# Performance work log

Measured on AMD Instinct MI355X. Metric: run time of the kernel, lower is better.

Reference implementation:

```python
import jax, jax.numpy as jnp
import numpy as np

N = 2048

def setup_inputs() -> dict:
    key = jax.random.key(0)
    k0, k1, k2, k3 = jax.random.split(key, 4)
    return {
        "input": jax.random.normal(k0, (N, N), dtype=jnp.float32),
        "weight1": jax.random.normal(k1, (N, N), dtype=jnp.float32),
        "weight2": jax.random.normal(k2, (N, N), dtype=jnp.float32),
        "weight3": jax.random.normal(k3, (N, N), dtype=jnp.float32),
    }

def reference(input, weight1, weight2, weight3):
    # Faithful translation of the torch DAG (duplicate mm kept: t4 == t2,
    # so t8 is mathematically zero, but we preserve the original math).
    t1 = input @ weight1
    t2 = input @ weight2
    t3 = weight3 @ weight3
    t4 = input @ weight2
    t5 = t1 * weight1
    t6 = (t5 @ input) * weight1
    t7 = t1 * t2 + t1 + t3
    t8 = t2 - t4
    t9 = t7 * t8 + t6 * t3
    t11 = t3 * t9
    t12 = t3 * (t1 @ input) * t6
    t13 = t7 + t11
    t14 = t8 + t12
    t15 = t13 + t14
    return t15
```

## Files before the change

### kernel.cpp

```cpp
#include <hip/hip_runtime.h>
#include <hip/hip_bf16.h>
#include <stdint.h>

#define NN 2048
#define BK 32

typedef __bf16 bf16;
typedef __bf16 bf16x8 __attribute__((ext_vector_type(8)));
typedef __bf16 bf16x4 __attribute__((ext_vector_type(4)));
typedef float f32x4 __attribute__((ext_vector_type(4)));

__device__ __forceinline__ void async_copy16(bf16* lds, const bf16* g) {
    __builtin_amdgcn_global_load_lds(
        (const __attribute__((address_space(1))) unsigned int*)g,
        (__attribute__((address_space(3))) unsigned int*)lds,
        16, 0, 0);
}

#define WAIT_VM(n) asm volatile("s_waitcnt vmcnt(" #n ")" ::: "memory")
#define BAR()                                  \
    do {                                       \
        asm volatile("" ::: "memory");         \
        __builtin_amdgcn_s_barrier();          \
        asm volatile("" ::: "memory");         \
    } while (0)

struct CastArgs {
    const float* in[4];
    bf16*        outT[4];
    bf16*        outN[4];
};

__global__ __launch_bounds__(256) void transpose_cast_kernel(CastArgs args) {
    const float* __restrict__ in = args.in[blockIdx.z];
    bf16* __restrict__ outT      = args.outT[blockIdx.z];
    bf16* __restrict__ outN      = args.outN[blockIdx.z];
    __shared__ float tile[64][65];
    const int bx = blockIdx.x * 64;
    const int by = blockIdx.y * 64;
    const int t  = threadIdx.x;
    const int tc = t & 15, tr = t >> 4;
#pragma unroll
    for (int p = 0; p < 4; ++p) {
        const int r = tr + p * 16;
        const float4 v = *(const float4*)&in[(size_t)(by + r) * NN + bx + tc * 4];
        tile[r][tc * 4 + 0] = v.x; tile[r][tc * 4 + 1] = v.y;
        tile[r][tc * 4 + 2] = v.z; tile[r][tc * 4 + 3] = v.w;
        if (outN) {
            bf16x4 b = {(bf16)v.x, (bf16)v.y, (bf16)v.z, (bf16)v.w};
            *(bf16x4*)&outN[(size_t)(by + r) * NN + bx + tc * 4] = b;
        }
    }
    __syncthreads();
    const int cc = t >> 2, e = t & 3;
#pragma unroll
    for (int u = 0; u < 2; ++u) {
        const int r0 = e * 16 + u * 8;
        bf16x8 b;
#pragma unroll
        for (int i = 0; i < 8; ++i) b[i] = (bf16)tile[r0 + i][cc];
        *(bf16x8*)&outT[(size_t)(bx + cc) * NN + by + r0] = b;
    }
}

struct Gemm3Args {
    const bf16*  A[3];
    const bf16*  Bt[3];
    float*       C[3];
    const float* W1;
    bf16*        M1bf;
    bf16*        B1bf;
};

__global__ __launch_bounds__(256) void gemm3_kernel(Gemm3Args args) {
    const bf16* __restrict__ A  = args.A[blockIdx.z];
    const bf16* __restrict__ Bt = args.Bt[blockIdx.z];
    float* __restrict__ C       = args.C[blockIdx.z];

    __shared__ bf16 As0[128 * BK], As1[128 * BK], As2[128 * BK];
    __shared__ bf16 Bs0[128 * BK], Bs1[128 * BK], Bs2[128 * BK];

    const int t  = threadIdx.x;
    const int bm = blockIdx.x * 128;
    const int bn = blockIdx.y * 128;

    const int row0 = t >> 2;
    const int qp   = t & 3;
    const int col0 = ((qp ^ ((row0 >> 1) & 3)) << 3);
    const int off0 = t * 8;

    const bf16* gA0 = A  + (size_t)(bm + row0) * NN + col0;
    const bf16* gB0 = Bt + (size_t)(bn + row0) * NN + col0;

    const int wave = t >> 6;
    const int lane = t & 63;
    const int wm   = (wave >> 1) * 64;
    const int wn   = (wave & 1) * 64;
    const int lrow = lane & 15;
    const int q    = lane >> 4;
    const int qe   = (q ^ ((lrow >> 1) & 3)) << 3;

    f32x4 acc[4][4];
#pragma unroll
    for (int i = 0; i < 4; ++i)
#pragma unroll
        for (int j = 0; j < 4; ++j) acc[i][j] = (f32x4){0.f, 0.f, 0.f, 0.f};

    auto issue = [&](bf16* As, bf16* Bs, int kt) {
        const int kof = kt * BK;
        async_copy16(&As[off0],           gA0 + kof);
        async_copy16(&As[off0 + 64 * BK], gA0 + (size_t)64 * NN + kof);
        async_copy16(&Bs[off0],           gB0 + kof);
        async_copy16(&Bs[off0 + 64 * BK], gB0 + (size_t)64 * NN + kof);
    };
    auto compute = [&](const bf16* As, const bf16* Bs) {
        bf16x8 af[4], bfr[4];
#pragma unroll
        for (int i = 0; i < 4; ++i)
            af[i] = *(const bf16x8*)&As[(wm + i * 16 + lrow) * BK + qe];
#pragma unroll
        for (int j = 0; j < 4; ++j)
            bfr[j] = *(const bf16x8*)&Bs[(wn + j * 16 + lrow) * BK + qe];
#pragma unroll
        for (int i = 0; i < 4; ++i)
#pragma unroll
            for (int j = 0; j < 4; ++j)
                acc[i][j] = __builtin_amdgcn_mfma_f32_16x16x32_bf16(
                    af[i], bfr[j], acc[i][j], 0, 0, 0);
    };

    issue(As0, Bs0, 0);
    issue(As1, Bs1, 1);
#pragma unroll 1
    for (int kt = 0; kt < 60; kt += 3) {
        issue(As2, Bs2, kt + 2); WAIT_VM(8); BAR(); compute(As0, Bs0); BAR();
        issue(As0, Bs0, kt + 3); WAIT_VM(8); BAR(); compute(As1, Bs1); BAR();
        issue(As1, Bs1, kt + 4); WAIT_VM(8); BAR(); compute(As2, Bs2); BAR();
    }
    issue(As2, Bs2, 62); WAIT_VM(8); BAR(); compute(As0, Bs0); BAR();
    issue(As0, Bs0, 63); WAIT_VM(8); BAR(); compute(As1, Bs1); BAR();
    WAIT_VM(4); BAR(); compute(As2, Bs2); BAR();
    WAIT_VM(0); BAR(); compute(As0, Bs0);

    const int z = blockIdx.z;
#pragma unroll
    for (int i = 0; i < 4; ++i)
#pragma unroll
        for (int j = 0; j < 4; ++j)
#pragma unroll
            for (int r = 0; r < 4; ++r) {
                const size_t idx = (size_t)(bm + wm + i * 16 + q * 4 + r) * NN +
                                   (bn + wn + j * 16 + lrow);
                const float v = acc[i][j][r];
                C[idx] = v;
                if (z == 0) {
                    const float w = args.W1[idx];
                    args.M1bf[idx] = (bf16)v;
                    args.B1bf[idx] = (bf16)(v * w);
                }
            }
}

struct Gemm2Args {
    const bf16*  M1bf;
    const bf16*  B1bf;
    const bf16*  At;
    const float* M1;
    const float* M3;
    const float* W1;
    float*       out;
};

__global__ __launch_bounds__(256) void gemm2_fused_kernel(Gemm2Args args) {
    __shared__ bf16 A50[128 * BK], A51[128 * BK], A52[128 * BK];
    __shared__ bf16 A40[128 * BK], A41[128 * BK], A42[128 * BK];
    __shared__ bf16 Bs0[64 * BK],  Bs1[64 * BK],  Bs2[64 * BK];

    const int t  = threadIdx.x;
    const int bm = blockIdx.x * 128;
    const int bn = blockIdx.y * 64;

    const int row0 = t >> 2;
    const int qp   = t & 3;
    const int col0 = ((qp ^ ((row0 >> 1) & 3)) << 3);
    const int off0 = t * 8;

    const bf16* g5 = args.M1bf + (size_t)(bm + row0) * NN + col0;
    const bf16* g4 = args.B1bf + (size_t)(bm + row0) * NN + col0;
    const bf16* gB = args.At   + (size_t)(bn + row0) * NN + col0;

    const int wave = t >> 6;
    const int lane = t & 63;
    const int wm   = (wave >> 1) * 64;
    const int wn   = (wave & 1) * 32;
    const int lrow = lane & 15;
    const int q    = lane >> 4;
    const int qe   = (q ^ ((lrow >> 1) & 3)) << 3;

    f32x4 acc5[4][2], acc4[4][2];
#pragma unroll
    for (int i = 0; i < 4; ++i)
#pragma unroll
        for (int j = 0; j < 2; ++j) {
            acc5[i][j] = (f32x4){0.f, 0.f, 0.f, 0.f};
            acc4[i][j] = (f32x4){0.f, 0.f, 0.f, 0.f};
        }

    auto issue = [&](bf16* A5, bf16* A4, bf16* Bs, int kt) {
        const int kof = kt * BK;
        async_copy16(&A5[off0],           g5 + kof);
        async_copy16(&A5[off0 + 64 * BK], g5 + (size_t)64 * NN + kof);
        async_copy16(&A4[off0],           g4 + kof);
        async_copy16(&A4[off0 + 64 * BK], g4 + (size_t)64 * NN + kof);
        async_copy16(&Bs[off0],           gB + kof);
    };
    auto compute = [&](const bf16* A5, const bf16* A4, const bf16* Bs) {
        bf16x8 a5[4], a4[4], bfr[2];
#pragma unroll
        for (int i = 0; i < 4; ++i) {
            a5[i] = *(const bf16x8*)&A5[(wm + i * 16 + lrow) * BK + qe];
            a4[i] = *(const bf16x8*)&A4[(wm + i * 16 + lrow) * BK + qe];
        }
#pragma unroll
        for (int j = 0; j < 2; ++j)
            bfr[j] = *(const bf16x8*)&Bs[(wn + j * 16 + lrow) * BK + qe];
#pragma unroll
        for (int i = 0; i < 4; ++i)
#pragma unroll
            for (int j = 0; j < 2; ++j) {
                acc5[i][j] = __builtin_amdgcn_mfma_f32_16x16x32_bf16(
                    a5[i], bfr[j], acc5[i][j], 0, 0, 0);
                acc4[i][j] = __builtin_amdgcn_mfma_f32_16x16x32_bf16(
                    a4[i], bfr[j], acc4[i][j], 0, 0, 0);
            }
    };

    issue(A50, A40, Bs0, 0);
    issue(A51, A41, Bs1, 1);
#pragma unroll 1
    for (int kt = 0; kt < 60; kt += 3) {
        issue(A52, A42, Bs2, kt + 2); WAIT_VM(10); BAR(); compute(A50, A40, Bs0); BAR();
        issue(A50, A40, Bs0, kt + 3); WAIT_VM(10); BAR(); compute(A51, A41, Bs1); BAR();
        issue(A51, A41, Bs1, kt + 4); WAIT_VM(10); BAR(); compute(A52, A42, Bs2); BAR();
    }
    issue(A52, A42, Bs2, 62); WAIT_VM(10); BAR(); compute(A50, A40, Bs0); BAR();
    issue(A50, A40, Bs0, 63); WAIT_VM(10); BAR(); compute(A51, A41, Bs1); BAR();
    WAIT_VM(5); BAR(); compute(A52, A42, Bs2); BAR();
    WAIT_VM(0); BAR(); compute(A50, A40, Bs0);

#pragma unroll
    for (int i = 0; i < 4; ++i)
#pragma unroll
        for (int j = 0; j < 2; ++j)
#pragma unroll
            for (int r = 0; r < 4; ++r) {
                const size_t idx = (size_t)(bm + wm + i * 16 + q * 4 + r) * NN +
                                   (bn + wn + j * 16 + lrow);
                const float m5 = acc5[i][j][r];
                const float m4 = acc4[i][j][r];
                const float m1 = args.M1[idx];
                const float m3 = args.M3[idx];
                const float w1 = args.W1[idx];
                const float m2 = args.out[idx];
                args.out[idx] =
                    m1 * m2 + m1 + m3 + m3 * (m4 * w1) * (m3 + m5);
            }
}

extern "C" void kernel_launch(void* const* d_in, const int* in_sizes, int n_in,
                              void* d_out, int out_size, void* d_ws, size_t ws_size,
                              hipStream_t stream) {
    const float* A  = (const float*)d_in[0];
    const float* W1 = (const float*)d_in[1];
    const float* W2 = (const float*)d_in[2];
    const float* W3 = (const float*)d_in[3];
    float* out = (float*)d_out;

    const size_t P = (size_t)NN * NN;
    char* ws = (char*)d_ws;

    bf16* Abf  = (bf16*)ws;
    bf16* At   = Abf + P;
    bf16* W1t  = At + P;
    bf16* W2t  = W1t + P;
    bf16* W3bf = W2t + P;
    bf16* W3t  = W3bf + P;
    bf16* M1bf = W3t + P;
    bf16* B1bf = M1bf + P;
    float* M1  = (float*)(B1bf + P);
    float* M3  = M1 + P;

    CastArgs ca;
    ca.in[0] = A;  ca.outT[0] = At;  ca.outN[0] = Abf;
    ca.in[1] = W1; ca.outT[1] = W1t; ca.outN[1] = nullptr;
    ca.in[2] = W2; ca.outT[2] = W2t; ca.outN[2] = nullptr;
    ca.in[3] = W3; ca.outT[3] = W3t; ca.outN[3] = W3bf;
    transpose_cast_kernel<<<dim3(NN / 64, NN / 64, 4), 256, 0, stream>>>(ca);

    Gemm3Args g3;
    g3.A[0] = Abf;  g3.Bt[0] = W1t; g3.C[0] = M1;
    g3.A[1] = Abf;  g3.Bt[1] = W2t; g3.C[1] = out;
    g3.A[2] = W3bf; g3.Bt[2] = W3t; g3.C[2] = M3;
    g3.W1 = W1; g3.M1bf = M1bf; g3.B1bf = B1bf;
    gemm3_kernel<<<dim3(NN / 128, NN / 128, 3), 256, 0, stream>>>(g3);

    Gemm2Args g2;
    g2.M1bf = M1bf; g2.B1bf = B1bf; g2.At = At;
    g2.M1 = M1; g2.M3 = M3; g2.W1 = W1; g2.out = out;
    gemm2_fused_kernel<<<dim3(NN / 128, NN / 64), 256, 0, stream>>>(g2);
}
```

Before: 258.6 us.

## Merge A@W1 and A@W2 GEMMs sharing A tiles; double-buffer and retile phase kernels

The first GEMM phase now computes input@W1 and input@W2 in one block, so each A tile loaded into LDS feeds two B operands. The W3@W3 product runs as a separate z-slice. Both paths move from triple to double buffering and request two blocks per CU via launch_bounds. The second fused GEMM gives each wave a 32x64 tile instead of 64x32, and the transpose-cast kernel changes its LDS read pattern on the transposed write side. This cuts A-tile global traffic but leaves the z=0 and z=1 blocks with unequal work (two accumulators versus one), which can cause load imbalance and higher register pressure.

```diff
diff --git a/kernel.cpp b/kernel.cpp
--- a/kernel.cpp
+++ b/kernel.cpp
@@ -39,46 +39,48 @@
     const int bx = blockIdx.x * 64;
     const int by = blockIdx.y * 64;
     const int t  = threadIdx.x;
-    const int tc = t & 15, tr = t >> 4;
+    const int c4 = (t & 15) * 4, r0 = t >> 4;
 #pragma unroll
     for (int p = 0; p < 4; ++p) {
-        const int r = tr + p * 16;
-        const float4 v = *(const float4*)&in[(size_t)(by + r) * NN + bx + tc * 4];
-        tile[r][tc * 4 + 0] = v.x; tile[r][tc * 4 + 1] = v.y;
-        tile[r][tc * 4 + 2] = v.z; tile[r][tc * 4 + 3] = v.w;
+        const int r = r0 + p * 16;
+        const float4 v = *(const float4*)&in[(size_t)(by + r) * NN + bx + c4];
+        tile[r][c4 + 0] = v.x; tile[r][c4 + 1] = v.y;
+        tile[r][c4 + 2] = v.z; tile[r][c4 + 3] = v.w;
         if (outN) {
             bf16x4 b = {(bf16)v.x, (bf16)v.y, (bf16)v.z, (bf16)v.w};
-            *(bf16x4*)&outN[(size_t)(by + r) * NN + bx + tc * 4] = b;
+            *(bf16x4*)&outN[(size_t)(by + r) * NN + bx + c4] = b;
         }
     }
     __syncthreads();
-    const int cc = t >> 2, e = t & 3;
-#pragma unroll
-    for (int u = 0; u < 2; ++u) {
-        const int r0 = e * 16 + u * 8;
+    const int cc8 = (t & 7) * 8, rw0 = t >> 3;
+#pragma unroll
+    for (int p = 0; p < 2; ++p) {
+        const int rw = rw0 + p * 32;
         bf16x8 b;
 #pragma unroll
-        for (int i = 0; i < 8; ++i) b[i] = (bf16)tile[r0 + i][cc];
-        *(bf16x8*)&outT[(size_t)(bx + cc) * NN + by + r0] = b;
+        for (int i = 0; i < 8; ++i) b[i] = (bf16)tile[cc8 + i][rw];
+        *(bf16x8*)&outT[(size_t)(bx + rw) * NN + by + cc8] = b;
     }
 }
 
-struct Gemm3Args {
-    const bf16*  A[3];
-    const bf16*  Bt[3];
-    float*       C[3];
+struct P1Args {
+    const bf16*  Abf;
+    const bf16*  W1t;
+    const bf16*  W2t;
+    const bf16*  W3bf;
+    const bf16*  W3t;
+    float*       M1;
+    float*       M2out;
+    float*       M3;
     const float* W1;
     bf16*        M1bf;
     bf16*        B1bf;
 };
 
-__global__ __launch_bounds__(256) void gemm3_kernel(Gemm3Args args) {
-    const bf16* __restrict__ A  = args.A[blockIdx.z];
-    const bf16* __restrict__ Bt = args.Bt[blockIdx.z];
-    float* __restrict__ C       = args.C[blockIdx.z];
-
-    __shared__ bf16 As0[128 * BK], As1[128 * BK], As2[128 * BK];
-    __shared__ bf16 Bs0[128 * BK], Bs1[128 * BK], Bs2[128 * BK];
+__global__ __launch_bounds__(256, 2) void phase1_kernel(P1Args a) {
+    __shared__ bf16 As0[128 * BK], As1[128 * BK];
+    __shared__ bf16 B10[128 * BK], B11[128 * BK];
+    __shared__ bf16 B20[128 * BK], B21[128 * BK];
 
     const int t  = threadIdx.x;
     const int bm = blockIdx.x * 128;
@@ -88,9 +90,6 @@
     const int qp   = t & 3;
     const int col0 = ((qp ^ ((row0 >> 1) & 3)) << 3);
     const int off0 = t * 8;
-
-    const bf16* gA0 = A  + (size_t)(bm + row0) * NN + col0;
-    const bf16* gB0 = Bt + (size_t)(bn + row0) * NN + col0;
 
     const int wave = t >> 6;
     const int lane = t & 63;
@@ -100,65 +99,134 @@
     const int q    = lane >> 4;
     const int qe   = (q ^ ((lrow >> 1) & 3)) << 3;
 
-    f32x4 acc[4][4];
-#pragma unroll
-    for (int i = 0; i < 4; ++i)
-#pragma unroll
-        for (int j = 0; j < 4; ++j) acc[i][j] = (f32x4){0.f, 0.f, 0.f, 0.f};
-
-    auto issue = [&](bf16* As, bf16* Bs, int kt) {
-        const int kof = kt * BK;
-        async_copy16(&As[off0],           gA0 + kof);
-        async_copy16(&As[off0 + 64 * BK], gA0 + (size_t)64 * NN + kof);
-        async_copy16(&Bs[off0],           gB0 + kof);
-        async_copy16(&Bs[off0 + 64 * BK], gB0 + (size_t)64 * NN + kof);
-    };
-    auto compute = [&](const bf16* As, const bf16* Bs) {
-        bf16x8 af[4], bfr[4];
+    if (blockIdx.z == 0) {
+        const bf16* gA  = a.Abf + (size_t)(bm + row0) * NN + col0;
+        const bf16* gB1 = a.W1t + (size_t)(bn + row0) * NN + col0;
+        const bf16* gB2 = a.W2t + (size_t)(bn + row0) * NN + col0;
+
+        f32x4 acc1[4][4], acc2[4][4];
 #pragma unroll
         for (int i = 0; i < 4; ++i)
-            af[i] = *(const bf16x8*)&As[(wm + i * 16 + lrow) * BK + qe];
-#pragma unroll
-        for (int j = 0; j < 4; ++j)
-            bfr[j] = *(const bf16x8*)&Bs[(wn + j * 16 + lrow) * BK + qe];
+#pragma unroll
+            for (int j = 0; j < 4; ++j) {
+                acc1[i][j] = (f32x4){0.f, 0.f, 0.f, 0.f};
+                acc2[i][j] = (f32x4){0.f, 0.f, 0.f, 0.f};
+            }
+
+        auto issue = [&](bf16* As, bf16* B1, bf16* B2, int kt) {
+            const int kof = kt * BK;
+            async_copy16(&As[off0],           gA  + kof);
+            async_copy16(&As[off0 + 64 * BK], gA  + (size_t)64 * NN + kof);
+            async_copy16(&B1[off0],           gB1 + kof);
+            async_copy16(&B1[off0 + 64 * BK], gB1 + (size_t)64 * NN + kof);
+            async_copy16(&B2[off0],           gB2 + kof);
+            async_copy16(&B2[off0 + 64 * BK], gB2 + (size_t)64 * NN + kof);
+        };
+        auto compute = [&](const bf16* As, const bf16* B1, const bf16* B2) {
+            bf16x8 af[4], b1[4], b2[4];
+#pragma unroll
+            for (int i = 0; i < 4; ++i)
+                af[i] = *(const bf16x8*)&As[(wm + i * 16 + lrow) * BK + qe];
+#pragma unroll
+            for (int j = 0; j < 4; ++j) {
+                b1[j] = *(const bf16x8*)&B1[(wn + j * 16 + lrow) * BK + qe];
+                b2[j] = *(const bf16x8*)&B2[(wn + j * 16 + lrow) * BK + qe];
+            }
+#pragma unroll
+            for (int i = 0; i < 4; ++i)
+#pragma unroll
+                for (int j = 0; j < 4; ++j) {
+                    acc1[i][j] = __builtin_amdgcn_mfma_f32_16x16x32_bf16(
+                        af[i], b1[j], acc1[i][j], 0, 0, 0);
+                    acc2[i][j] = __builtin_amdgcn_mfma_f32_16x16x32_bf16(
+                        af[i], b2[j], acc2[i][j], 0, 0, 0);
+                }
+        };
+
+        issue(As0, B10, B20, 0);
+#pragma unroll 1
+        for (int kt = 0; kt < 62; kt += 2) {
+            issue(As1, B11, B21, kt + 1); WAIT_VM(6); BAR();
+            compute(As0, B10, B20); BAR();
+            issue(As0, B10, B20, kt + 2); WAIT_VM(6); BAR();
+            compute(As1, B11, B21); BAR();
+        }
+        issue(As1, B11, B21, 63); WAIT_VM(6); BAR();
+        compute(As0, B10, B20); BAR();
+        WAIT_VM(0); BAR();
+        compute(As1, B11, B21);
+
 #pragma unroll
         for (int i = 0; i < 4; ++i)
 #pragma unroll
             for (int j = 0; j < 4; ++j)
-                acc[i][j] = __builtin_amdgcn_mfma_f32_16x16x32_bf16(
-                    af[i], bfr[j], acc[i][j], 0, 0, 0);
-    };
-
-    issue(As0, Bs0, 0);
-    issue(As1, Bs1, 1);
+#pragma unroll
+                for (int r = 0; r < 4; ++r) {
+                    const size_t idx =
+                        (size_t)(bm + wm + i * 16 + q * 4 + r) * NN +
+                        (bn + wn + j * 16 + lrow);
+                    const float v1 = acc1[i][j][r];
+                    a.M1[idx]    = v1;
+                    a.M2out[idx] = acc2[i][j][r];
+                    const float w = a.W1[idx];
+                    a.M1bf[idx] = (bf16)v1;
+                    a.B1bf[idx] = (bf16)(v1 * w);
+                }
+    } else {
+        const bf16* gA = a.W3bf + (size_t)(bm + row0) * NN + col0;
+        const bf16* gB = a.W3t  + (size_t)(bn + row0) * NN + col0;
+
+        f32x4 acc[4][4];
+#pragma unroll
+        for (int i = 0; i < 4; ++i)
+#pragma unroll
+            for (int j = 0; j < 4; ++j) acc[i][j] = (f32x4){0.f, 0.f, 0.f, 0.f};
+
+        auto issue = [&](bf16* As, bf16* Bs, int kt) {
+            const int kof = kt * BK;
+            async_copy16(&As[off0],           gA + kof);
+            async_copy16(&As[off0 + 64 * BK], gA + (size_t)64 * NN + kof);
+            async_copy16(&Bs[off0],           gB + kof);
+            async_copy16(&Bs[off0 + 64 * BK], gB + (size_t)64 * NN + kof);
+        };
+        auto compute = [&](const bf16* As, const bf16* Bs) {
+            bf16x8 af[4], bfr[4];
+#pragma unroll
+            for (int i = 0; i < 4; ++i)
+                af[i] = *(const bf16x8*)&As[(wm + i * 16 + lrow) * BK + qe];
+#pragma unroll
+            for (int j = 0; j < 4; ++j)
+                bfr[j] = *(const bf16x8*)&Bs[(wn + j * 16 + lrow) * BK + qe];
+#pragma unroll
+            for (int i = 0; i < 4; ++i)
+#pragma unroll
+                for (int j = 0; j < 4; ++j)
+                    acc[i][j] = __builtin_amdgcn_mfma_f32_16x16x32_bf16(
+                        af[i], bfr[j], acc[i][j], 0, 0, 0);
+        };
+
+        issue(As0, B10, 0);
 #pragma unroll 1
-    for (int kt = 0; kt < 60; kt += 3) {
-        issue(As2, Bs2, kt + 2); WAIT_VM(8); BAR(); compute(As0, Bs0); BAR();
-        issue(As0, Bs0, kt + 3); WAIT_VM(8); BAR(); compute(As1, Bs1); BAR();
-        issue(As1, Bs1, kt + 4); WAIT_VM(8); BAR(); compute(As2, Bs2); BAR();
+        for (int kt = 0; kt < 62; kt += 2) {
+            issue(As1, B11, kt + 1); WAIT_VM(4); BAR();
+            compute(As0, B10); BAR();
+            issue(As0, B10, kt + 2); WAIT_VM(4); BAR();
+            compute(As1, B11); BAR();
+        }
+        issue(As1, B11, 63); WAIT_VM(4); BAR();
+        compute(As0, B10); BAR();
+        WAIT_VM(0); BAR();
+        compute(As1, B11);
+
+#pragma unroll
+        for (int i = 0; i < 4; ++i)
+#pragma unroll
+            for (int j = 0; j < 4; ++j)
+#pragma unroll
+                for (int r = 0; r < 4; ++r)
+                    a.M3[(size_t)(bm + wm + i * 16 + q * 4 + r) * NN +
+                         (bn + wn + j * 16 + lrow)] = acc[i][j][r];
     }
-    issue(As2, Bs2, 62); WAIT_VM(8); BAR(); compute(As0, Bs0); BAR();
-    issue(As0, Bs0, 63); WAIT_VM(8); BAR(); compute(As1, Bs1); BAR();
-    WAIT_VM(4); BAR(); compute(As2, Bs2); BAR();
-    WAIT_VM(0); BAR(); compute(As0, Bs0);
-
-    const int z = blockIdx.z;
-#pragma unroll
-    for (int i = 0; i < 4; ++i)
-#pragma unroll
-        for (int j = 0; j < 4; ++j)
-#pragma unroll
-            for (int r = 0; r < 4; ++r) {
-                const size_t idx = (size_t)(bm + wm + i * 16 + q * 4 + r) * NN +
-                                   (bn + wn + j * 16 + lrow);
-                const float v = acc[i][j][r];
-                C[idx] = v;
-                if (z == 0) {
-                    const float w = args.W1[idx];
-                    args.M1bf[idx] = (bf16)v;
-                    args.B1bf[idx] = (bf16)(v * w);
-                }
-            }
 }
 
 struct Gemm2Args {
@@ -171,7 +239,7 @@
     float*       out;
 };
 
-__global__ __launch_bounds__(256) void gemm2_fused_kernel(Gemm2Args args) {
+__global__ __launch_bounds__(256, 2) void gemm2_fused_kernel(Gemm2Args args) {
     __shared__ bf16 A50[128 * BK], A51[128 * BK], A52[128 * BK];
     __shared__ bf16 A40[128 * BK], A41[128 * BK], A42[128 * BK];
     __shared__ bf16 Bs0[64 * BK],  Bs1[64 * BK],  Bs2[64 * BK];
@@ -191,17 +259,16 @@
 
     const int wave = t >> 6;
     const int lane = t & 63;
-    const int wm   = (wave >> 1) * 64;
-    const int wn   = (wave & 1) * 32;
+    const int wm   = wave * 32;
     const int lrow = lane & 15;
     const int q    = lane >> 4;
     const int qe   = (q ^ ((lrow >> 1) & 3)) << 3;
 
-    f32x4 acc5[4][2], acc4[4][2];
-#pragma unroll
-    for (int i = 0; i < 4; ++i)
-#pragma unroll
-        for (int j = 0; j < 2; ++j) {
+    f32x4 acc5[2][4], acc4[2][4];
+#pragma unroll
+    for (int i = 0; i < 2; ++i)
+#pragma unroll
+        for (int j = 0; j < 4; ++j) {
             acc5[i][j] = (f32x4){0.f, 0.f, 0.f, 0.f};
             acc4[i][j] = (f32x4){0.f, 0.f, 0.f, 0.f};
         }
@@ -215,19 +282,19 @@
         async_copy16(&Bs[off0],           gB + kof);
     };
     auto compute = [&](const bf16* A5, const bf16* A4, const bf16* Bs) {
-        bf16x8 a5[4], a4[4], bfr[2];
-#pragma unroll
-        for (int i = 0; i < 4; ++i) {
+        bf16x8 a5[2], a4[2], bfr[4];
+#pragma unroll
+        for (int i = 0; i < 2; ++i) {
             a5[i] = *(const bf16x8*)&A5[(wm + i * 16 + lrow) * BK + qe];
             a4[i] = *(const bf16x8*)&A4[(wm + i * 16 + lrow) * BK + qe];
         }
 #pragma unroll
-        for (int j = 0; j < 2; ++j)
-            bfr[j] = *(const bf16x8*)&Bs[(wn + j * 16 + lrow) * BK + qe];
-#pragma unroll
-        for (int i = 0; i < 4; ++i)
-#pragma unroll
-            for (int j = 0; j < 2; ++j) {
+        for (int j = 0; j < 4; ++j)
+            bfr[j] = *(const bf16x8*)&Bs[(j * 16 + lrow) * BK + qe];
+#pragma unroll
+        for (int i = 0; i < 2; ++i)
+#pragma unroll
+            for (int j = 0; j < 4; ++j) {
                 acc5[i][j] = __builtin_amdgcn_mfma_f32_16x16x32_bf16(
                     a5[i], bfr[j], acc5[i][j], 0, 0, 0);
                 acc4[i][j] = __builtin_amdgcn_mfma_f32_16x16x32_bf16(
@@ -249,13 +316,13 @@
     WAIT_VM(0); BAR(); compute(A50, A40, Bs0);
 
 #pragma unroll
-    for (int i = 0; i < 4; ++i)
-#pragma unroll
-        for (int j = 0; j < 2; ++j)
+    for (int i = 0; i < 2; ++i)
+#pragma unroll
+        for (int j = 0; j < 4; ++j)
 #pragma unroll
             for (int r = 0; r < 4; ++r) {
                 const size_t idx = (size_t)(bm + wm + i * 16 + q * 4 + r) * NN +
-                                   (bn + wn + j * 16 + lrow);
+                                   (bn + j * 16 + lrow);
                 const float m5 = acc5[i][j][r];
                 const float m4 = acc4[i][j][r];
                 const float m1 = args.M1[idx];
@@ -297,12 +364,11 @@
     ca.in[3] = W3; ca.outT[3] = W3t; ca.outN[3] = W3bf;
     transpose_cast_kernel<<<dim3(NN / 64, NN / 64, 4), 256, 0, stream>>>(ca);
 
-    Gemm3Args g3;
-    g3.A[0] = Abf;  g3.Bt[0] = W1t; g3.C[0] = M1;
-    g3.A[1] = Abf;  g3.Bt[1] = W2t; g3.C[1] = out;
-    g3.A[2] = W3bf; g3.Bt[2] = W3t; g3.C[2] = M3;
-    g3.W1 = W1; g3.M1bf = M1bf; g3.B1bf = B1bf;
-    gemm3_kernel<<<dim3(NN / 128, NN / 128, 3), 256, 0, stream>>>(g3);
+    P1Args p1;
+    p1.Abf = Abf; p1.W1t = W1t; p1.W2t = W2t; p1.W3bf = W3bf; p1.W3t = W3t;
+    p1.M1 = M1; p1.M2out = out; p1.M3 = M3;
+    p1.W1 = W1; p1.M1bf = M1bf; p1.B1bf = B1bf;
+    phase1_kernel<<<dim3(NN / 128, NN / 128, 2), 256, 0, stream>>>(p1);
 
     Gemm2Args g2;
     g2.M1bf = M1bf; g2.B1bf = B1bf; g2.At = At;
```

Measured after the change: 232.4 us. -10.1%, faster.
